# Kernel tuning notes

Measured on AMD Instinct MI355X. Metric: run time of the kernel, lower is better.

## Reference

```python
import jax, jax.numpy as jnp
import numpy as np

B, C, H, W = 32, 256, 32, 32
N_EMBED = 8192
BETA = 0.25  # used for the (unreturned) commitment loss in the original


def setup_inputs() -> dict:
    key = jax.random.key(0)
    k1, k2 = jax.random.split(key)
    z = jax.random.normal(k1, (B, C, H, W), dtype=jnp.float32)
    embedding = jax.random.normal(k2, (N_EMBED, C), dtype=jnp.float32)
    return {"z": z, "embedding": embedding}


def reference(z, embedding):
    # z: [b, c, h, w] -> [b, h, w, c] -> [N, d]
    b, c, h, w = z.shape
    z_bhwc = jnp.transpose(z, (0, 2, 3, 1))
    z_flat = z_bhwc.reshape(-1, c)  # [N, d]

    # Squared L2 distance to every codebook entry: [N, n_embed]
    d = (
        jnp.sum(z_flat * z_flat, axis=1, keepdims=True)
        + jnp.sum(embedding * embedding, axis=1)
        - 2.0 * jnp.einsum("nd,kd->nk", z_flat, embedding)
    )
    min_encoding_indices = jnp.argmin(d, axis=1)  # [N] int

    # Codebook gather + straight-through estimator
    z_q = embedding[min_encoding_indices].reshape(b, h, w, c)
    z_q = z_bhwc + jax.lax.stop_gradient(z_q - z_bhwc)
    z_q = jnp.transpose(z_q, (0, 3, 1, 2))  # back to [b, c, h, w]
    return z_q, min_encoding_indices
```

## Files before the change

### kernel.cpp

```cpp
#include <hip/hip_runtime.h>

#define BATCH   32
#define CDIM    256
#define HWSZ    1024
#define NTOK    32768
#define KEMB    8192
#define ZQ_SIZE (BATCH * CDIM * HWSZ)

typedef short bf16x8 __attribute__((ext_vector_type(8)));
typedef float floatx4 __attribute__((ext_vector_type(4)));

#define MSPLIT 4
#define STRIP  (KEMB / MSPLIT)
#define MB8    128
#define NB8    128
#define MT8    (STRIP / MB8)

#define WS8_ESQ   0ULL
#define WS8_EQM   32768ULL
#define WS8_EH    65536ULL
#define WS8_ZH    4259840ULL
#define WS8_ZL    21037056ULL
#define WS8_PART  37814272ULL
#define WS8_IDX   39911424ULL
#define WS8_TOTAL 40042496ULL

__device__ __forceinline__ unsigned short bf16rne(float f) {
    unsigned int u = __float_as_uint(f);
    return (unsigned short)((u + 0x7fffu + ((u >> 16) & 1u)) >> 16);
}
__device__ __forceinline__ unsigned int packsplit(float f) {
    unsigned int u  = __float_as_uint(f);
    unsigned int hi = (u + 0x7fffu + ((u >> 16) & 1u)) >> 16;
    float rest      = f - __uint_as_float(hi << 16);
    unsigned int u2 = __float_as_uint(rest);
    unsigned int lo = (u2 + 0x7fffu + ((u2 >> 16) & 1u)) >> 16;
    return (hi << 16) | lo;
}
__device__ __forceinline__ unsigned umin32(unsigned a, unsigned b) { return a < b ? a : b; }
__device__ __forceinline__ unsigned umax32(unsigned a, unsigned b) { return a > b ? a : b; }

#define GLOAD_LDS16(g, l) \
    __builtin_amdgcn_global_load_lds((const __attribute__((address_space(1))) void*)(g), \
                                     (__attribute__((address_space(3))) void*)(l), 16, 0, 0)

__global__ void esqcvt_kernel(const float* __restrict__ emb, float* __restrict__ eSq,
                              float* __restrict__ eqm, unsigned short* __restrict__ eh) {
    int k    = blockIdx.x * 4 + (threadIdx.x >> 6);
    int lane = threadIdx.x & 63;
    float4 v = *(const float4*)&emb[k * CDIM + lane * 4];
    float s  = v.x * v.x + v.y * v.y + v.z * v.z + v.w * v.w;
    #pragma unroll
    for (int off = 32; off; off >>= 1) s += __shfl_down(s, off);
    ushort4 h = make_ushort4(bf16rne(v.x), bf16rne(v.y), bf16rne(v.z), bf16rne(v.w));
    *(ushort4*)&eh[k * CDIM + lane * 4] = h;
    if (lane == 0) { eSq[k] = s; eqm[k] = s * 2048.0f + 8388608.0f; }
}

__global__ void splitz_kernel(const float* __restrict__ z, unsigned short* __restrict__ zh,
                              unsigned short* __restrict__ zl) {
    __shared__ unsigned int tile[64][65];
    int b  = blockIdx.x >> 6;
    int r  = blockIdx.x & 63;
    int dt = r >> 4, ht = r & 15;
    int t  = threadIdx.x;
    #pragma unroll
    for (int i = 0; i < 4; ++i) {
        int u  = t + 256 * i;
        int dr = u >> 4;
        int c4 = (u & 15) * 4;
        float4 v = *(const float4*)&z[(((size_t)(b * 256 + dt * 64 + dr)) << 10) + ht * 64 + c4];
        tile[dr][c4 + 0] = packsplit(v.x);
        tile[dr][c4 + 1] = packsplit(v.y);
        tile[dr][c4 + 2] = packsplit(v.z);
        tile[dr][c4 + 3] = packsplit(v.w);
    }
    __syncthreads();
    #pragma unroll
    for (int i = 0; i < 2; ++i) {
        int u  = t + 256 * i;
        int tr = u & 63;
        int d8 = u >> 6;
        unsigned short h8[8], l8[8];
        #pragma unroll
        for (int j = 0; j < 8; ++j) {
            unsigned int p = tile[d8 * 8 + j][tr];
            h8[j] = (unsigned short)(p >> 16);
            l8[j] = (unsigned short)(p & 0xffff);
        }
        size_t off = (size_t)(b * 1024 + ht * 64 + tr) * 256 + dt * 64 + d8 * 8;
        *(uint4*)&zh[off] = *(uint4*)h8;
        *(uint4*)&zl[off] = *(uint4*)l8;
    }
}

__global__ __launch_bounds__(256, 2)
void dist8_kernel(const unsigned short* __restrict__ zhp,
                  const unsigned short* __restrict__ ehp,
                  const float* __restrict__ eqm,
                  uint4* __restrict__ part) {
    __shared__ __align__(16) char lds[65536];

    const int t    = threadIdx.x;
    const int lane = t & 63;
    const int wv   = t >> 6;
    const int wm   = wv >> 1, wn = wv & 1;
    const int l15  = lane & 15, quad = lane >> 4;

    const int nb = blockIdx.x & 255;
    const int q  = blockIdx.x >> 8;
    const int n0 = nb * NB8;
    const int cstrip = q * STRIP;

    const int dmaRow  = lane >> 3;
    const int dmaChnk = (lane & 7) ^ dmaRow;
    const unsigned laneGoff = (unsigned)dmaRow * 512 + (unsigned)dmaChnk * 16;

    const char* gA0 = (const char*)ehp + (size_t)(cstrip + wv * 32) * 512 + laneGoff;
    const char* gB0 = (const char*)zhp + (size_t)(n0 + wv * 32) * 512 + laneGoff;
    const unsigned wvOff = (unsigned)wv * 4096;
    const unsigned cx = (unsigned)(l15 & 7);

    #pragma unroll
    for (int dr = 0; dr < 4; ++dr)
        #pragma unroll
        for (int j = 0; j < 4; ++j)
            GLOAD_LDS16(gB0 + dr * 128 + j * 4096, lds + dr * 16384 + wvOff + j * 1024);
    __syncthreads();

    bf16x8 bfr[4][4][2];
    #pragma unroll
    for (int cf = 0; cf < 4; ++cf) {
        const unsigned bRow = (unsigned)(wn * 64 + cf * 16 + l15) * 128;
        #pragma unroll
        for (int dr = 0; dr < 4; ++dr)
            #pragma unroll
            for (int dk = 0; dk < 2; ++dk)
                bfr[cf][dr][dk] = *(const bf16x8*)(lds + (unsigned)dr * 16384 + bRow +
                                    (((unsigned)(dk * 4) + (unsigned)quad) ^ cx) * 16);
    }
    __syncthreads();

    unsigned aR[4];
    #pragma unroll
    for (int rf = 0; rf < 4; ++rf) aR[rf] = (unsigned)(wm * 64 + rf * 16 + l15) * 128;

    unsigned k1[4], k2[4], k3[4];
    #pragma unroll
    for (int cf = 0; cf < 4; ++cf) { k1[cf] = 0xFFFFFFFFu; k2[cf] = 0xFFFFFFFFu; k3[cf] = 0xFFFFFFFFu; }

    #pragma unroll
    for (int j = 0; j < 4; ++j)
        GLOAD_LDS16(gA0 + j * 4096, lds + wvOff + j * 1024);

    int r = 0;
    for (int mt = 0; mt < MT8; ++mt) {
        floatx4 acc[4][4];
        #pragma unroll
        for (int rf = 0; rf < 4; ++rf)
            #pragma unroll
            for (int cf = 0; cf < 4; ++cf) acc[rf][cf] = (floatx4){0.f, 0.f, 0.f, 0.f};

        #pragma unroll
        for (int dr = 0; dr < 4; ++dr, ++r) {
            __syncthreads();
            if (r + 1 < 4 * MT8) {
                const int rn  = r + 1;
                const int mtn = rn >> 2, drn = rn & 3;
                const unsigned bon = (unsigned)(rn & 1) << 14;
                const char* ga = gA0 + (size_t)mtn * 65536 + drn * 128;
                #pragma unroll
                for (int j = 0; j < 4; ++j)
                    GLOAD_LDS16(ga + j * 4096, lds + bon + wvOff + j * 1024);
            }
            const unsigned bo = (unsigned)(r & 1) << 14;
            #pragma unroll
            for (int dk = 0; dk < 2; ++dk) {
                const unsigned xoff = bo + (((unsigned)(dk * 4) + (unsigned)quad) ^ cx) * 16;
                bf16x8 afr[4];
                #pragma unroll
                for (int rf = 0; rf < 4; ++rf) afr[rf] = *(const bf16x8*)(lds + aR[rf] + xoff);
                #pragma unroll
                for (int rf = 0; rf < 4; ++rf)
                    #pragma unroll
                    for (int cf = 0; cf < 4; ++cf)
                        acc[rf][cf] = __builtin_amdgcn_mfma_f32_16x16x32_bf16(afr[rf], bfr[cf][dr][dk], acc[rf][cf], 0, 0, 0);
            }
        }

        #pragma unroll
        for (int rf = 0; rf < 4; ++rf) {
            const int kb = cstrip + mt * MB8 + wm * 64 + rf * 16 + quad * 4;
            floatx4 eq = *(const floatx4*)&eqm[kb];
            const unsigned lb = (unsigned)(mt * MB8 + wm * 64 + rf * 16 + quad * 4);
            #pragma unroll
            for (int cf = 0; cf < 4; ++cf) {
                #pragma unroll
                for (int rr = 0; rr < 4; ++rr) {
                    float kf = fmaf(acc[rf][cf][rr], -4096.f, eq[rr]);
                    unsigned key = (__float_as_uint(kf) << 11) | (lb + (unsigned)rr);
                    unsigned m1 = umax32(k1[cf], key);
                    k1[cf] = umin32(k1[cf], key);
                    unsigned m2 = umax32(k2[cf], m1);
                    k2[cf] = umin32(k2[cf], m1);
                    k3[cf] = umin32(k3[cf], m2);
                }
            }
        }
    }

    #pragma unroll
    for (int cf = 0; cf < 4; ++cf) {
        #pragma unroll
        for (int s = 0; s < 2; ++s) {
            int m = s ? 32 : 16;
            unsigned o1 = (unsigned)__shfl((int)k1[cf], lane ^ m, 64);
            unsigned o2 = (unsigned)__shfl((int)k2[cf], lane ^ m, 64);
            unsigned o3 = (unsigned)__shfl((int)k3[cf], lane ^ m, 64);
            unsigned a1  = umax32(k1[cf], o1);
            k1[cf]       = umin32(k1[cf], o1);
            unsigned b1  = umin32(k2[cf], o2);
            unsigned r3a = umax32(a1, b1);
            k2[cf]       = umin32(a1, b1);
            k3[cf]       = umin32(r3a, umin32(k3[cf], o3));
        }
    }

    __syncthreads();
    uint4* red = (uint4*)lds;
    if (quad == 0) {
        #pragma unroll
        for (int cf = 0; cf < 4; ++cf)
            red[wm * 128 + wn * 64 + cf * 16 + l15] = make_uint4(k1[cf], k2[cf], k3[cf], 0u);
    }
    __syncthreads();
    if (t < 128) {
        uint4 a = red[t], b = red[128 + t];
        unsigned a1  = umax32(a.x, b.x);
        unsigned r1  = umin32(a.x, b.x);
        unsigned b1  = umin32(a.y, b.y);
        unsigned r3a = umax32(a1, b1);
        unsigned r2  = umin32(a1, b1);
        unsigned r3  = umin32(r3a, umin32(a.z, b.z));
        part[q * NTOK + n0 + t] = make_uint4(r1, r2, r3, 0u);
    }
}

__global__ void rescore12_kernel(const unsigned short* __restrict__ zh,
                                 const unsigned short* __restrict__ zl,
                                 const float* __restrict__ emb,
                                 const float* __restrict__ eSq, const uint4* __restrict__ part,
                                 int* __restrict__ idx, float* __restrict__ idxF) {
    int n    = blockIdx.x * 4 + (threadIdx.x >> 6);
    int lane = threadIdx.x & 63;
    int c[12];
    #pragma unroll
    for (int s = 0; s < 4; ++s) {
        uint4 p = part[s * NTOK + n];
        c[3 * s]     = s * STRIP + (int)(p.x & 0x7FFu);
        c[3 * s + 1] = s * STRIP + (int)(p.y & 0x7FFu);
        c[3 * s + 2] = s * STRIP + (int)(p.z & 0x7FFu);
    }
    ushort4 h = *(const ushort4*)&zh[(size_t)n * CDIM + lane * 4];
    ushort4 l = *(const ushort4*)&zl[(size_t)n * CDIM + lane * 4];
    float z0 = __uint_as_float((unsigned)h.x << 16) + __uint_as_float((unsigned)l.x << 16);
    float z1 = __uint_as_float((unsigned)h.y << 16) + __uint_as_float((unsigned)l.y << 16);
    float z2 = __uint_as_float((unsigned)h.z << 16) + __uint_as_float((unsigned)l.z << 16);
    float z3 = __uint_as_float((unsigned)h.w << 16) + __uint_as_float((unsigned)l.w << 16);
    float acc[12];
    #pragma unroll
    for (int s = 0; s < 12; ++s) {
        float4 e = *(const float4*)&emb[(size_t)c[s] * CDIM + lane * 4];
        acc[s] = fmaf(z0, e.x, fmaf(z1, e.y, fmaf(z2, e.z, z3 * e.w)));
    }
    #pragma unroll
    for (int off = 32; off; off >>= 1) {
        #pragma unroll
        for (int s = 0; s < 12; ++s) acc[s] += __shfl_down(acc[s], off);
    }
    if (lane == 0) {
        float bd = 3.4e38f; int bi = 0x7fffffff;
        #pragma unroll
        for (int s = 0; s < 12; ++s) {
            float dv = eSq[c[s]] - 2.f * acc[s];
            if (dv < bd || (dv == bd && c[s] < bi)) { bd = dv; bi = c[s]; }
        }
        idx[n]  = bi;
        idxF[n] = (float)bi;
    }
}

__global__ void gather2_kernel(const float* __restrict__ emb, const int* __restrict__ idx,
                               float* __restrict__ out) {
    __shared__ float tile[32 * 260];
    __shared__ int rows[32];
    const int t  = threadIdx.x;
    const int n0 = blockIdx.x * 32;
    if (t < 32) rows[t] = idx[n0 + t];
    __syncthreads();
    {
        int r  = t >> 3;
        int c0 = (t & 7) * 32;
        const float* src = emb + (size_t)rows[r] * CDIM + c0;
        #pragma unroll
        for (int j = 0; j < 8; ++j) {
            float4 v = *(const float4*)(src + j * 4);
            *(float4*)&tile[r * 260 + c0 + j * 4] = v;
        }
    }
    __syncthreads();
    const int b   = n0 >> 10;
    const int hw0 = n0 & 1023;
    const int cg  = t >> 3;
    const int h4  = (t & 7) * 4;
    #pragma unroll
    for (int j = 0; j < 8; ++j) {
        int c = cg + j * 32;
        float4 v;
        v.x = tile[(h4 + 0) * 260 + c];
        v.y = tile[(h4 + 1) * 260 + c];
        v.z = tile[(h4 + 2) * 260 + c];
        v.w = tile[(h4 + 3) * 260 + c];
        *(float4*)&out[((size_t)b << 18) | ((size_t)c << 10) | (size_t)(hw0 + h4)] = v;
    }
}

#define F_BM  128
#define F_BK  128
#define F_BD  32
#define F_BSS (F_BK + 4)
#define F_KSPLIT 4
#define F_KPER  (KEMB / F_KSPLIT)
#define FWS_ESQ 0
#define FWS_PV  32768
#define FWS_PI  557056
#define FWS_IDX 1081344

__global__ void esq_kernel(const float* __restrict__ emb, float* __restrict__ eSq) {
    int k    = blockIdx.x * 4 + (threadIdx.x >> 6);
    int lane = threadIdx.x & 63;
    float4 v = *(const float4*)&emb[k * CDIM + lane * 4];
    float s  = v.x * v.x + v.y * v.y + v.z * v.z + v.w * v.w;
    #pragma unroll
    for (int off = 32; off; off >>= 1) s += __shfl_down(s, off);
    if (lane == 0) eSq[k] = s;
}

__global__ void dist_kernel(const float* __restrict__ z, const float* __restrict__ emb,
                            const float* __restrict__ eSq,
                            float* __restrict__ pv, int* __restrict__ pi) {
    __shared__ __align__(16) char smem[(F_BD * F_BM + F_BD * F_BSS) * 4];
    float (*As)[F_BM]  = (float (*)[F_BM])smem;
    float (*Bs)[F_BSS] = (float (*)[F_BSS])(smem + F_BD * F_BM * 4);
    const int t = threadIdx.x, tx = t & 15, ty = t >> 4;
    const int rb = blockIdx.x & 255, q = blockIdx.x >> 8;
    const int m0 = rb * F_BM, bb = m0 >> 10, hw0 = m0 & 1023;
    float minv[8]; int mini[8];
    #pragma unroll
    for (int i = 0; i < 8; ++i) { minv[i] = 3.4028235e38f; mini[i] = 0; }
    const int kbeg = q * F_KPER;
    for (int k0 = kbeg; k0 < kbeg + F_KPER; k0 += F_BK) {
        float acc[8][8];
        #pragma unroll
        for (int r = 0; r < 8; ++r)
            #pragma unroll
            for (int c = 0; c < 8; ++c) acc[r][c] = 0.f;
        for (int d0 = 0; d0 < CDIM; d0 += F_BD) {
            __syncthreads();
            #pragma unroll
            for (int i = 0; i < 4; ++i) {
                int u = t + i * 256; int m4 = (u & 31) << 2; int cR = u >> 5;
                float4 v = *(const float4*)&z[(bb << 18) + ((d0 + cR) << 10) + hw0 + m4];
                *(float4*)&As[cR][m4] = v;
            }
            #pragma unroll
            for (int i = 0; i < 4; ++i) {
                int u = t + i * 256; int kR = u >> 3; int c4 = (u & 7) << 2;
                float4 v = *(const float4*)&emb[(k0 + kR) * CDIM + d0 + c4];
                Bs[c4 + 0][kR] = v.x; Bs[c4 + 1][kR] = v.y;
                Bs[c4 + 2][kR] = v.z; Bs[c4 + 3][kR] = v.w;
            }
            __syncthreads();
            #pragma unroll
            for (int d = 0; d < F_BD; ++d) {
                float a[8], bb2[8];
                *(float4*)&a[0] = *(const float4*)&As[d][(ty << 2)];
                *(float4*)&a[4] = *(const float4*)&As[d][64 + (ty << 2)];
                *(float4*)&bb2[0] = *(const float4*)&Bs[d][(tx << 2)];
                *(float4*)&bb2[4] = *(const float4*)&Bs[d][64 + (tx << 2)];
                #pragma unroll
                for (int r = 0; r < 8; ++r)
                    #pragma unroll
                    for (int c = 0; c < 8; ++c) acc[r][c] = fmaf(a[r], bb2[c], acc[r][c]);
            }
        }
        #pragma unroll
        for (int c = 0; c < 8; ++c) {
            int kk = (c < 4) ? ((tx << 2) + c) : (64 + (tx << 2) + (c - 4));
            int kg = k0 + kk;
            float es = eSq[kg];
            #pragma unroll
            for (int r = 0; r < 8; ++r) {
                float v = fmaf(-2.f, acc[r][c], es);
                if (v < minv[r]) { minv[r] = v; mini[r] = kg; }
            }
        }
    }
    __syncthreads();
    float (*redV)[16] = (float (*)[16])smem;
    int   (*redI)[16] = (int   (*)[16])(smem + F_BM * 16 * 4);
    #pragma unroll
    for (int r = 0; r < 8; ++r) {
        int row = (r < 4) ? ((ty << 2) + r) : (64 + (ty << 2) + (r - 4));
        redV[row][tx] = minv[r]; redI[row][tx] = mini[r];
    }
    __syncthreads();
    if (t < F_BM) {
        float bv = redV[t][0]; int bi = redI[t][0];
        #pragma unroll
        for (int i = 1; i < 16; ++i) {
            float v = redV[t][i]; int ii = redI[t][i];
            if (v < bv || (v == bv && ii < bi)) { bv = v; bi = ii; }
        }
        int n = m0 + t;
        pv[q * NTOK + n] = bv; pi[q * NTOK + n] = bi;
    }
}

__global__ void merge_kernel(const float* __restrict__ pv, const int* __restrict__ pi,
                             int* __restrict__ idxOut, float* __restrict__ idxFOut) {
    int n = blockIdx.x * 256 + threadIdx.x;
    float bv = pv[n]; int bi = pi[n];
    #pragma unroll
    for (int q = 1; q < F_KSPLIT; ++q) {
        float v = pv[q * NTOK + n]; int ii = pi[q * NTOK + n];
        if (v < bv || (v == bv && ii < bi)) { bv = v; bi = ii; }
    }
    idxOut[n] = bi; idxFOut[n] = (float)bi;
}

extern "C" void kernel_launch(void* const* d_in, const int* in_sizes, int n_in,
                              void* d_out, int out_size, void* d_ws, size_t ws_size,
                              hipStream_t stream) {
    const float* z   = (const float*)d_in[0];
    const float* emb = (const float*)d_in[1];
    float* out = (float*)d_out;
    char*  ws  = (char*)d_ws;

    if (ws_size >= WS8_TOTAL) {
        float*          eSq  = (float*)(ws + WS8_ESQ);
        float*          eqm  = (float*)(ws + WS8_EQM);
        unsigned short* eh   = (unsigned short*)(ws + WS8_EH);
        unsigned short* zh   = (unsigned short*)(ws + WS8_ZH);
        unsigned short* zl   = (unsigned short*)(ws + WS8_ZL);
        uint4*          part = (uint4*)(ws + WS8_PART);
        int*            idx  = (int*)(ws + WS8_IDX);

        esqcvt_kernel <<<KEMB / 4, 256, 0, stream>>>(emb, eSq, eqm, eh);
        splitz_kernel <<<2048, 256, 0, stream>>>(z, zh, zl);
        dist8_kernel  <<<256 * MSPLIT, 256, 0, stream>>>(zh, eh, eqm, part);
        rescore12_kernel<<<NTOK / 4, 256, 0, stream>>>(zh, zl, emb, eSq, part, idx, out + ZQ_SIZE);
        gather2_kernel<<<NTOK / 32, 256, 0, stream>>>(emb, idx, out);
    } else {
        float* eSq = (float*)(ws + FWS_ESQ);
        float* pv  = (float*)(ws + FWS_PV);
        int*   pi  = (int*)(ws + FWS_PI);
        int*   idx = (int*)(ws + FWS_IDX);
        esq_kernel  <<<KEMB / 4, 256, 0, stream>>>(emb, eSq);
        dist_kernel <<<256 * F_KSPLIT, 256, 0, stream>>>(z, emb, eSq, pv, pi);
        merge_kernel<<<NTOK / 256, 256, 0, stream>>>(pv, pi, idx, out + ZQ_SIZE);
        gather2_kernel<<<NTOK / 32, 256, 0, stream>>>(emb, idx, out);
    }
}
```

Before: 291.3 us.

## Triple-buffer codebook tiles with explicit vmcnt waits and stage eqm in LDS

Replaces the double-buffered A-tile pipeline, which used a full __syncthreads each round, with a three-slot ring. Two rounds are prefetched ahead, and partial vmcnt(4) waits plus raw s_barrier are used so one load group stays in flight during the MFMA round. The MFMA blocks are wrapped in s_setprio, and the per-strip codebook norms are loaded into LDS once instead of being read from global memory in each epilogue. LDS shrinks from 64KB to 56KB, and the B fragments are loaded in two halves to fit. The hand-written waitcnt logic depends on how many loads the compiler emits, so a miscount could cause races.

```diff
diff --git a/kernel.cpp b/kernel.cpp
--- a/kernel.cpp
+++ b/kernel.cpp
@@ -94,12 +94,63 @@
     }
 }
 
+#define EQOFF 49152u
+
+#define ISSUE_A(rn, bo_) do { \
+    const char* ga_ = gA0 + (size_t)((rn) >> 2) * 65536 + (size_t)((rn) & 3) * 128; \
+    _Pragma("unroll") \
+    for (int j_ = 0; j_ < 4; ++j_) \
+        GLOAD_LDS16(ga_ + j_ * 4096, lds + (bo_) + wvOff + j_ * 1024); \
+} while (0)
+
+#define MFMA_ROUND(dr_, bo_) do { \
+    __builtin_amdgcn_s_setprio(1); \
+    _Pragma("unroll") \
+    for (int dk_ = 0; dk_ < 2; ++dk_) { \
+        const unsigned xoff_ = (bo_) + (((unsigned)(dk_ * 4) + (unsigned)quad) ^ cx) * 16; \
+        bf16x8 afr_[4]; \
+        _Pragma("unroll") \
+        for (int rf_ = 0; rf_ < 4; ++rf_) afr_[rf_] = *(const bf16x8*)(lds + aR[rf_] + xoff_); \
+        _Pragma("unroll") \
+        for (int rf_ = 0; rf_ < 4; ++rf_) \
+            _Pragma("unroll") \
+            for (int cf_ = 0; cf_ < 4; ++cf_) \
+                acc[rf_][cf_] = __builtin_amdgcn_mfma_f32_16x16x32_bf16(afr_[rf_], bfr[cf_][dr_][dk_], acc[rf_][cf_], 0, 0, 0); \
+    } \
+    __builtin_amdgcn_s_setprio(0); \
+} while (0)
+
+#define TOP3_EPI(mt_) do { \
+    _Pragma("unroll") \
+    for (int rf_ = 0; rf_ < 4; ++rf_) { \
+        const unsigned base_ = (unsigned)((mt_) * MB8 + wm * 64 + rf_ * 16 + quad * 4); \
+        floatx4 eq = *(const floatx4*)(lds + EQOFF + (base_ << 2)); \
+        _Pragma("unroll") \
+        for (int cf_ = 0; cf_ < 4; ++cf_) { \
+            _Pragma("unroll") \
+            for (int rr_ = 0; rr_ < 4; ++rr_) { \
+                float kf = fmaf(acc[rf_][cf_][rr_], -4096.f, eq[rr_]); \
+                unsigned key = (__float_as_uint(kf) << 11) | (base_ + (unsigned)rr_); \
+                unsigned m1 = umax32(k1[cf_], key); \
+                k1[cf_] = umin32(k1[cf_], key); \
+                unsigned m2 = umax32(k2[cf_], m1); \
+                k2[cf_] = umin32(k2[cf_], m1); \
+                k3[cf_] = umin32(k3[cf_], m2); \
+            } \
+        } \
+    } \
+} while (0)
+
+#define VMW4()  asm volatile("s_waitcnt vmcnt(4)" ::: "memory")
+#define VMW0()  asm volatile("s_waitcnt vmcnt(0)" ::: "memory")
+#define BARR()  asm volatile("s_barrier" ::: "memory")
+
 __global__ __launch_bounds__(256, 2)
 void dist8_kernel(const unsigned short* __restrict__ zhp,
                   const unsigned short* __restrict__ ehp,
                   const float* __restrict__ eqm,
                   uint4* __restrict__ part) {
-    __shared__ __align__(16) char lds[65536];
+    __shared__ __align__(16) char lds[57344];
 
     const int t    = threadIdx.x;
     const int lane = t & 63;
@@ -121,25 +172,46 @@
     const unsigned wvOff = (unsigned)wv * 4096;
     const unsigned cx = (unsigned)(l15 & 7);
 
-    #pragma unroll
-    for (int dr = 0; dr < 4; ++dr)
+    bf16x8 bfr[4][4][2];
+
+    #pragma unroll
+    for (int s = 0; s < 2; ++s)
         #pragma unroll
         for (int j = 0; j < 4; ++j)
-            GLOAD_LDS16(gB0 + dr * 128 + j * 4096, lds + dr * 16384 + wvOff + j * 1024);
-    __syncthreads();
-
-    bf16x8 bfr[4][4][2];
+            GLOAD_LDS16(gB0 + s * 128 + j * 4096, lds + s * 16384 + wvOff + j * 1024);
+    #pragma unroll
+    for (int j = 0; j < 2; ++j)
+        GLOAD_LDS16((const char*)(eqm + cstrip) + wv * 2048 + j * 1024 + lane * 16,
+                    lds + EQOFF + (unsigned)wv * 2048 + (unsigned)j * 1024);
+    __syncthreads();
     #pragma unroll
     for (int cf = 0; cf < 4; ++cf) {
         const unsigned bRow = (unsigned)(wn * 64 + cf * 16 + l15) * 128;
         #pragma unroll
-        for (int dr = 0; dr < 4; ++dr)
+        for (int s = 0; s < 2; ++s)
             #pragma unroll
             for (int dk = 0; dk < 2; ++dk)
-                bfr[cf][dr][dk] = *(const bf16x8*)(lds + (unsigned)dr * 16384 + bRow +
+                bfr[cf][s][dk] = *(const bf16x8*)(lds + s * 16384 + bRow +
                                     (((unsigned)(dk * 4) + (unsigned)quad) ^ cx) * 16);
     }
     __syncthreads();
+    #pragma unroll
+    for (int s = 0; s < 2; ++s)
+        #pragma unroll
+        for (int j = 0; j < 4; ++j)
+            GLOAD_LDS16(gB0 + (s + 2) * 128 + j * 4096, lds + s * 16384 + wvOff + j * 1024);
+    __syncthreads();
+    #pragma unroll
+    for (int cf = 0; cf < 4; ++cf) {
+        const unsigned bRow = (unsigned)(wn * 64 + cf * 16 + l15) * 128;
+        #pragma unroll
+        for (int s = 0; s < 2; ++s)
+            #pragma unroll
+            for (int dk = 0; dk < 2; ++dk)
+                bfr[cf][s + 2][dk] = *(const bf16x8*)(lds + s * 16384 + bRow +
+                                    (((unsigned)(dk * 4) + (unsigned)quad) ^ cx) * 16);
+    }
+    __syncthreads();
 
     unsigned aR[4];
     #pragma unroll
@@ -149,12 +221,11 @@
     #pragma unroll
     for (int cf = 0; cf < 4; ++cf) { k1[cf] = 0xFFFFFFFFu; k2[cf] = 0xFFFFFFFFu; k3[cf] = 0xFFFFFFFFu; }
 
-    #pragma unroll
-    for (int j = 0; j < 4; ++j)
-        GLOAD_LDS16(gA0 + j * 4096, lds + wvOff + j * 1024);
-
-    int r = 0;
-    for (int mt = 0; mt < MT8; ++mt) {
+    ISSUE_A(0, 0u);
+    ISSUE_A(1, 16384u);
+
+    unsigned bufR = 0u;
+    for (int mt = 0; mt < MT8 - 1; ++mt) {
         floatx4 acc[4][4];
         #pragma unroll
         for (int rf = 0; rf < 4; ++rf)
@@ -162,51 +233,41 @@
             for (int cf = 0; cf < 4; ++cf) acc[rf][cf] = (floatx4){0.f, 0.f, 0.f, 0.f};
 
         #pragma unroll
-        for (int dr = 0; dr < 4; ++dr, ++r) {
-            __syncthreads();
-            if (r + 1 < 4 * MT8) {
-                const int rn  = r + 1;
-                const int mtn = rn >> 2, drn = rn & 3;
-                const unsigned bon = (unsigned)(rn & 1) << 14;
-                const char* ga = gA0 + (size_t)mtn * 65536 + drn * 128;
-                #pragma unroll
-                for (int j = 0; j < 4; ++j)
-                    GLOAD_LDS16(ga + j * 4096, lds + bon + wvOff + j * 1024);
-            }
-            const unsigned bo = (unsigned)(r & 1) << 14;
-            #pragma unroll
-            for (int dk = 0; dk < 2; ++dk) {
-                const unsigned xoff = bo + (((unsigned)(dk * 4) + (unsigned)quad) ^ cx) * 16;
-                bf16x8 afr[4];
-                #pragma unroll
-                for (int rf = 0; rf < 4; ++rf) afr[rf] = *(const bf16x8*)(lds + aR[rf] + xoff);
-                #pragma unroll
-                for (int rf = 0; rf < 4; ++rf)
-                    #pragma unroll
-                    for (int cf = 0; cf < 4; ++cf)
-                        acc[rf][cf] = __builtin_amdgcn_mfma_f32_16x16x32_bf16(afr[rf], bfr[cf][dr][dk], acc[rf][cf], 0, 0, 0);
-            }
-        }
-
-        #pragma unroll
-        for (int rf = 0; rf < 4; ++rf) {
-            const int kb = cstrip + mt * MB8 + wm * 64 + rf * 16 + quad * 4;
-            floatx4 eq = *(const floatx4*)&eqm[kb];
-            const unsigned lb = (unsigned)(mt * MB8 + wm * 64 + rf * 16 + quad * 4);
-            #pragma unroll
-            for (int cf = 0; cf < 4; ++cf) {
-                #pragma unroll
-                for (int rr = 0; rr < 4; ++rr) {
-                    float kf = fmaf(acc[rf][cf][rr], -4096.f, eq[rr]);
-                    unsigned key = (__float_as_uint(kf) << 11) | (lb + (unsigned)rr);
-                    unsigned m1 = umax32(k1[cf], key);
-                    k1[cf] = umin32(k1[cf], key);
-                    unsigned m2 = umax32(k2[cf], m1);
-                    k2[cf] = umin32(k2[cf], m1);
-                    k3[cf] = umin32(k3[cf], m2);
-                }
-            }
-        }
+        for (int dr = 0; dr < 4; ++dr) {
+            VMW4();
+            BARR();
+            const unsigned bufI = (bufR == 0u) ? 32768u : bufR - 16384u;
+            ISSUE_A(mt * 4 + dr + 2, bufI);
+            MFMA_ROUND(dr, bufR);
+            bufR = (bufR == 32768u) ? 0u : bufR + 16384u;
+        }
+        TOP3_EPI(mt);
+    }
+    {
+        floatx4 acc[4][4];
+        #pragma unroll
+        for (int rf = 0; rf < 4; ++rf)
+            #pragma unroll
+            for (int cf = 0; cf < 4; ++cf) acc[rf][cf] = (floatx4){0.f, 0.f, 0.f, 0.f};
+
+        VMW4(); BARR();
+        { const unsigned bufI = (bufR == 0u) ? 32768u : bufR - 16384u; ISSUE_A(62, bufI); }
+        MFMA_ROUND(0, bufR);
+        bufR = (bufR == 32768u) ? 0u : bufR + 16384u;
+
+        VMW4(); BARR();
+        { const unsigned bufI = (bufR == 0u) ? 32768u : bufR - 16384u; ISSUE_A(63, bufI); }
+        MFMA_ROUND(1, bufR);
+        bufR = (bufR == 32768u) ? 0u : bufR + 16384u;
+
+        VMW4(); BARR();
+        MFMA_ROUND(2, bufR);
+        bufR = (bufR == 32768u) ? 0u : bufR + 16384u;
+
+        VMW0(); BARR();
+        MFMA_ROUND(3, bufR);
+
+        TOP3_EPI(15);
     }
 
     #pragma unroll
```

After: 273.9 us. -6.0%, faster.
